# Performance work log

Measured on AMD Instinct MI355X. Metric: run time of the kernel, lower is better.

## Reference

```python
import jax, jax.numpy as jnp
import numpy as np

CANVAS_SIZE = 224
N_SEGMENTS = 4
N_SAMPLES = 50
SOFTNESS = 0.02


def setup_inputs() -> dict:
    key = jax.random.key(0)
    k1, k2 = jax.random.split(key)
    n_paths = 1024
    paths_control_points = jax.random.uniform(k1, (n_paths, N_SEGMENTS, 4, 2), dtype=jnp.float32)
    colors = jax.random.uniform(k2, (n_paths, 4), dtype=jnp.float32)
    return {"paths_control_points": paths_control_points, "colors": colors}


def reference(paths_control_points, colors):
    H = W = CANVAS_SIZE
    n_paths = paths_control_points.shape[0]

    # Cubic Bezier basis at t in linspace(0,1,50)[:-1]  -> (49, 4)
    t = jnp.linspace(0.0, 1.0, N_SAMPLES)[:-1]
    mt = 1.0 - t
    basis = jnp.stack([mt**3, 3.0 * mt**2 * t, 3.0 * mt * t**2, t**3], axis=-1)

    # Sample all curve points for all paths/segments at once: (P, S, T, 2)
    pts = jnp.einsum('tc,psce->pste', basis, paths_control_points)
    pts = pts.reshape(n_paths, -1, 2)  # (P, S*T, 2) == (P, 196, 2)

    center = pts.mean(axis=1)  # (P, 2) -> (x, y)
    avg_radius = jnp.linalg.norm(pts - center[:, None, :], axis=-1).mean(axis=1)  # (P,)

    # Pixel grid in [0,1], 'ij' indexing: grid_y varies over rows, grid_x over cols
    lin = jnp.linspace(0.0, 1.0, H)
    grid_y, grid_x = jnp.meshgrid(lin, lin, indexing='ij')  # (H, W) each

    # Distance field per path: (P, H, W)
    dx = grid_x[None] - center[:, 0, None, None]
    dy = grid_y[None] - center[:, 1, None, None]
    dist = jnp.sqrt(dx * dx + dy * dy)

    # Soft disk mask scaled by per-path alpha: (P, H, W)
    masks = jax.nn.sigmoid((avg_radius[:, None, None] - dist) / SOFTNESS)
    masks = masks * colors[:, 3, None, None]

    # Sequential front-to-back alpha compositing (order matters) via scan
    canvas0 = jnp.ones((3, H, W), dtype=paths_control_points.dtype)

    def step(canvas, xs):
        m, c = xs  # m: (H, W), c: (3,)
        canvas = canvas * (1.0 - m)[None] + c[:, None, None] * m[None]
        return canvas, None

    canvas, _ = jax.lax.scan(step, canvas0, (masks, colors[:, :3]))
    return canvas
```

## Files before the change

kernel.cpp:

```cpp
#include <hip/hip_runtime.h>
#include <math.h>

#define NPATHS   1024
#define CANVAS_H 224
#define CANVAS_W 224
#define NPIX     (CANVAS_H * CANVAS_W)
#define NSAMP    49
#define K2EXP    72.134752f
#define CULL_MARGIN 0.22f

#define NWAVES   8
#define PPW      (NPATHS / NWAVES)


typedef __attribute__((ext_vector_type(16))) int   i16x16;
typedef __attribute__((ext_vector_type(2)))  float f32x2;

__device__ __forceinline__ float sf(int v) { return __int_as_float(v); }

__global__ __launch_bounds__(256) void path_setup_kernel(
    const float* __restrict__ cps,
    const float* __restrict__ colors,
    float* __restrict__ pd)
{
    const int tid = blockIdx.x * 256 + threadIdx.x;
    const int p = tid >> 2;
    const int s = tid & 3;

    const float4* cp4 = reinterpret_cast<const float4*>(cps);
    float4 a = cp4[p * 8 + s * 2];
    float4 b = cp4[p * 8 + s * 2 + 1];

    float sx = 0.0f, sy = 0.0f;
    for (int i = 0; i < NSAMP; ++i) {
        float t  = (float)i * (1.0f / 49.0f);
        float mt = 1.0f - t;
        float b0 = mt * mt * mt;
        float b1 = 3.0f * mt * mt * t;
        float b2 = 3.0f * mt * t * t;
        float b3 = t * t * t;
        sx += b0 * a.x + b1 * a.z + b2 * b.x + b3 * b.z;
        sy += b0 * a.y + b1 * a.w + b2 * b.y + b3 * b.w;
    }
    sx += __shfl_xor(sx, 1); sx += __shfl_xor(sx, 2);
    sy += __shfl_xor(sy, 1); sy += __shfl_xor(sy, 2);
    const float inv_n = 1.0f / 196.0f;
    float cx = sx * inv_n;
    float cy = sy * inv_n;

    float sr = 0.0f;
    for (int i = 0; i < NSAMP; ++i) {
        float t  = (float)i * (1.0f / 49.0f);
        float mt = 1.0f - t;
        float b0 = mt * mt * mt;
        float b1 = 3.0f * mt * mt * t;
        float b2 = 3.0f * mt * t * t;
        float b3 = t * t * t;
        float ptx = b0 * a.x + b1 * a.z + b2 * b.x + b3 * b.z;
        float pty = b0 * a.y + b1 * a.w + b2 * b.y + b3 * b.w;
        float dx = ptx - cx;
        float dy = pty - cy;
        sr += sqrtf(dx * dx + dy * dy);
    }
    sr += __shfl_xor(sr, 1); sr += __shfl_xor(sr, 2);
    float r = sr * inv_n;

    if (s == 0) {
        float4 col = reinterpret_cast<const float4*>(colors)[p];
        float rc = r + CULL_MARGIN;
        float4* o = reinterpret_cast<float4*>(pd) + (size_t)p * 2;
        o[0] = make_float4(cx, cy, -K2EXP * r, col.w);
        o[1] = make_float4(col.x * col.w, col.y * col.w, col.z * col.w, rc * rc);
    }
}

__global__ __launch_bounds__(512) void render_kernel(
    const float* __restrict__ pd,
    float* __restrict__ out)
{
    __shared__ float4 xch[NWAVES * 64];

    const int wave = __builtin_amdgcn_readfirstlane((int)(threadIdx.x >> 6));
    const int lane = threadIdx.x & 63;
    const int lx = lane & 7;
    const int ly = lane >> 3;
    const int xx = blockIdx.x * 8 + lx;
    const int yy = blockIdx.y * 8 + ly;

    f32x2 pxy;
    pxy.x = (float)xx * (1.0f / 223.0f);
    pxy.y = (float)yy * (1.0f / 223.0f);

    const float* wptr = pd + (size_t)wave * (PPW * 8);

    float T = 1.0f, Ab = 0.0f;
    f32x2 ra; ra.x = 0.0f; ra.y = 0.0f;

    for (int p = 0; p < PPW / 2; ++p) {
        i16x16 blk;
        asm volatile("s_load_dwordx16 %0, %1, 0x0\n\ts_waitcnt lgkmcnt(0)"
                     : "=s"(blk)
                     : "s"(wptr + p * 16));
#pragma unroll
        for (int j = 0; j < 2; ++j) {
            const int o = j * 8;
            f32x2 cxy;
            cxy.x = sf(blk[o + 0]);
            cxy.y = sf(blk[o + 1]);
            float c2  = sf(blk[o + 2]);
            float al  = sf(blk[o + 3]);
            float rr  = sf(blk[o + 7]);

            f32x2 dxy = pxy - cxy;
            f32x2 sq  = dxy * dxy;
            float d2  = sq.x + sq.y;
            if (__any(d2 < rr)) {
                float dist = __builtin_amdgcn_sqrtf(d2);
                float e = __builtin_amdgcn_exp2f(__builtin_fmaf(dist, K2EXP, c2));
                float q = __builtin_amdgcn_rcpf(1.0f + e);
                float om = __builtin_fmaf(-al, q, 1.0f);

                f32x2 crg;
                crg.x = sf(blk[o + 4]);
                crg.y = sf(blk[o + 5]);
                float cba = sf(blk[o + 6]);

                f32x2 om2; om2.x = om; om2.y = om;
                ra = ra * om2 + crg * (f32x2){q, q};
                T  = T * om;
                Ab = __builtin_fmaf(Ab, om, cba * q);
            }
        }
    }

    xch[wave * 64 + lane] = make_float4(T, ra.x, ra.y, Ab);
    __syncthreads();

    if (wave == 0) {
        float R = 1.0f, G = 1.0f, B = 1.0f;
#pragma unroll
        for (int w = 0; w < NWAVES; ++w) {
            float4 c = xch[w * 64 + lane];
            R = __builtin_fmaf(R, c.x, c.y);
            G = __builtin_fmaf(G, c.x, c.z);
            B = __builtin_fmaf(B, c.x, c.w);
        }
        const int pix = yy * CANVAS_W + xx;
        out[pix]            = R;
        out[NPIX + pix]     = G;
        out[2 * NPIX + pix] = B;
    }
}

extern "C" void kernel_launch(void* const* d_in, const int* in_sizes, int n_in,
                              void* d_out, int out_size, void* d_ws, size_t ws_size,
                              hipStream_t stream) {
    const float* cps    = (const float*)d_in[0];
    const float* colors = (const float*)d_in[1];
    float* out = (float*)d_out;
    float* pd  = (float*)d_ws;

    path_setup_kernel<<<(NPATHS * 4) / 256, 256, 0, stream>>>(cps, colors, pd);

    dim3 grid(CANVAS_W / 8, CANVAS_H / 8);
    render_kernel<<<grid, 512, 0, stream>>>(pd, out);
}
```

Before: 42.56 us.

## Double-buffer scalar path loads and drop per-wave radius culling branch

Replaces the per-iteration blocking scalar load with a two-buffer software pipeline, so the next 16-dword path block is fetched while the current two paths are composited. It also removes the wave-level cull test (`__any(d2 < rr)`) and its margin, so every path is now shaded for every pixel without branching. This aims to hide scalar-load latency and remove branch and vote overhead. The cost is that work previously skipped for distant paths is now always computed.

```diff
diff --git a/kernel.cpp b/kernel.cpp
--- a/kernel.cpp
+++ b/kernel.cpp
@@ -7,7 +7,6 @@
 #define NPIX     (CANVAS_H * CANVAS_W)
 #define NSAMP    49
 #define K2EXP    72.134752f
-#define CULL_MARGIN 0.22f
 
 #define NWAVES   8
 #define PPW      (NPATHS / NWAVES)
@@ -67,10 +66,9 @@
 
     if (s == 0) {
         float4 col = reinterpret_cast<const float4*>(colors)[p];
-        float rc = r + CULL_MARGIN;
         float4* o = reinterpret_cast<float4*>(pd) + (size_t)p * 2;
         o[0] = make_float4(cx, cy, -K2EXP * r, col.w);
-        o[1] = make_float4(col.x * col.w, col.y * col.w, col.z * col.w, rc * rc);
+        o[1] = make_float4(col.x * col.w, col.y * col.w, col.z * col.w, 0.0f);
     }
 }
 
@@ -96,59 +94,66 @@
     float T = 1.0f, Ab = 0.0f;
     f32x2 ra; ra.x = 0.0f; ra.y = 0.0f;
 
-    for (int p = 0; p < PPW / 2; ++p) {
-        i16x16 blk;
-        asm volatile("s_load_dwordx16 %0, %1, 0x0\n\ts_waitcnt lgkmcnt(0)"
-                     : "=s"(blk)
-                     : "s"(wptr + p * 16));
-#pragma unroll
-        for (int j = 0; j < 2; ++j) {
-            const int o = j * 8;
-            f32x2 cxy;
-            cxy.x = sf(blk[o + 0]);
-            cxy.y = sf(blk[o + 1]);
-            float c2  = sf(blk[o + 2]);
-            float al  = sf(blk[o + 3]);
-            float rr  = sf(blk[o + 7]);
+#define BODY(blk, j)                                                       \
+    {                                                                      \
+        const int o = (j) * 8;                                             \
+        f32x2 cxy;                                                         \
+        cxy.x = sf(blk[o + 0]);                                            \
+        cxy.y = sf(blk[o + 1]);                                            \
+        float c2  = sf(blk[o + 2]);                                        \
+        float al  = sf(blk[o + 3]);                                        \
+        f32x2 dxy = pxy - cxy;                                             \
+        float d2  = __builtin_fmaf(dxy.x, dxy.x, dxy.y * dxy.y);           \
+        float dist = __builtin_amdgcn_sqrtf(d2);                           \
+        float e = __builtin_amdgcn_exp2f(__builtin_fmaf(dist, K2EXP, c2)); \
+        float q = __builtin_amdgcn_rcpf(1.0f + e);                         \
+        float om = __builtin_fmaf(-al, q, 1.0f);                           \
+        f32x2 crg;                                                         \
+        crg.x = sf(blk[o + 4]);                                            \
+        crg.y = sf(blk[o + 5]);                                            \
+        float cba = sf(blk[o + 6]);                                        \
+        f32x2 om2; om2.x = om; om2.y = om;                                 \
+        f32x2 q2;  q2.x = q;   q2.y = q;                                   \
+        ra = ra * om2 + crg * q2;                                          \
+        T  = T * om;                                                       \
+        Ab = __builtin_fmaf(Ab, om, cba * q);                              \
+    }
 
-            f32x2 dxy = pxy - cxy;
-            f32x2 sq  = dxy * dxy;
-            float d2  = sq.x + sq.y;
-            if (__any(d2 < rr)) {
-                float dist = __builtin_amdgcn_sqrtf(d2);
-                float e = __builtin_amdgcn_exp2f(__builtin_fmaf(dist, K2EXP, c2));
-                float q = __builtin_amdgcn_rcpf(1.0f + e);
-                float om = __builtin_fmaf(-al, q, 1.0f);
+    i16x16 A, B;
+    asm volatile("s_load_dwordx16 %0, %1, 0x0" : "=s"(A) : "s"(wptr));
+    asm volatile("s_waitcnt lgkmcnt(0)" : "+s"(A));
 
-                f32x2 crg;
-                crg.x = sf(blk[o + 4]);
-                crg.y = sf(blk[o + 5]);
-                float cba = sf(blk[o + 6]);
-
-                f32x2 om2; om2.x = om; om2.y = om;
-                ra = ra * om2 + crg * (f32x2){q, q};
-                T  = T * om;
-                Ab = __builtin_fmaf(Ab, om, cba * q);
-            }
-        }
+    for (int i = 0; i < PPW / 4; ++i) {
+        asm volatile("s_load_dwordx16 %0, %1, 0x0"
+                     : "=s"(B) : "s"(wptr + (size_t)(2 * i + 1) * 16));
+        BODY(A, 0)
+        BODY(A, 1)
+        asm volatile("s_waitcnt lgkmcnt(0)" : "+s"(B));
+        if (i < PPW / 4 - 1)
+            asm volatile("s_load_dwordx16 %0, %1, 0x0"
+                         : "=s"(A) : "s"(wptr + (size_t)(2 * i + 2) * 16));
+        BODY(B, 0)
+        BODY(B, 1)
+        asm volatile("s_waitcnt lgkmcnt(0)" : "+s"(A));
     }
+#undef BODY
 
     xch[wave * 64 + lane] = make_float4(T, ra.x, ra.y, Ab);
     __syncthreads();
 
     if (wave == 0) {
-        float R = 1.0f, G = 1.0f, B = 1.0f;
+        float R = 1.0f, G = 1.0f, B2 = 1.0f;
 #pragma unroll
         for (int w = 0; w < NWAVES; ++w) {
             float4 c = xch[w * 64 + lane];
-            R = __builtin_fmaf(R, c.x, c.y);
-            G = __builtin_fmaf(G, c.x, c.z);
-            B = __builtin_fmaf(B, c.x, c.w);
+            R  = __builtin_fmaf(R,  c.x, c.y);
+            G  = __builtin_fmaf(G,  c.x, c.z);
+            B2 = __builtin_fmaf(B2, c.x, c.w);
         }
         const int pix = yy * CANVAS_W + xx;
         out[pix]            = R;
         out[NPIX + pix]     = G;
-        out[2 * NPIX + pix] = B;
+        out[2 * NPIX + pix] = B2;
     }
 }
 
```

After: 47.83 us. +12.4%, slower.
